# Kernel optimization log

Hardware: AMD Instinct MI355X
Metric: run time of the kernel (lower is better)

The kernel has to match this reference:

```python
import jax, jax.numpy as jnp
import numpy as np

D_MODEL, D_INNER, D_STATE, D_CONV = 1024, 2048, 16, 4
LN_EPS = 1e-5


def setup_inputs() -> dict:
    key = jax.random.key(0)
    ks = jax.random.split(key, 8)
    B, T = 2, 1024
    s = 0.02
    A = jnp.broadcast_to(jnp.arange(1, D_STATE + 1, dtype=jnp.float32), (D_INNER, D_STATE))
    return {
        "x": jax.random.normal(ks[0], (B, T, D_MODEL), jnp.float32),
        "ln_gamma": jnp.ones((D_MODEL,), jnp.float32),
        "ln_beta": jnp.zeros((D_MODEL,), jnp.float32),
        "W_in": jax.random.normal(ks[1], (2 * D_INNER, D_MODEL), jnp.float32) * s,
        "conv_w": jax.random.normal(ks[2], (D_INNER, D_CONV), jnp.float32) * s,
        "conv_b": jnp.zeros((D_INNER,), jnp.float32),
        "W_x": jax.random.normal(ks[3], (2 * D_STATE + 1, D_INNER), jnp.float32) * s,
        "w_dt": jax.random.normal(ks[4], (D_INNER, 1), jnp.float32) * s,
        "b_dt": jnp.zeros((D_INNER,), jnp.float32),
        "A_log": jnp.log(A),
        "D_param": jnp.ones((D_INNER,), jnp.float32),
        "W_out": jax.random.normal(ks[5], (D_MODEL, D_INNER), jnp.float32) * s,
    }


def _mamba_forward(x, ln_gamma, ln_beta, W_in, conv_w, conv_b, W_x, w_dt, b_dt, A_log, D_param, W_out):
    residual = x
    B, T, _ = x.shape
    # LayerNorm
    mu = x.mean(-1, keepdims=True)
    var = ((x - mu) ** 2).mean(-1, keepdims=True)
    xn = (x - mu) / jnp.sqrt(var + LN_EPS) * ln_gamma + ln_beta
    # in_proj -> split into x branch and gate z
    xz = xn @ W_in.T                       # [B,T,2*d_inner]
    xb, z = jnp.split(xz, 2, axis=-1)
    # depthwise causal conv1d (torch pad=d_conv-1, truncated to T == left pad)
    xp = jnp.pad(xb, ((0, 0), (D_CONV - 1, 0), (0, 0)))
    xc = conv_b + sum(xp[:, k:k + T, :] * conv_w[:, k] for k in range(D_CONV))
    xc = jax.nn.silu(xc)                   # [B,T,d_inner]
    # ssm parameter projections
    ssm_p = xc @ W_x.T                     # [B,T,2*d_state+1]
    dt_raw = ssm_p[..., :1]
    Bp = ssm_p[..., 1:1 + D_STATE]
    Cp = ssm_p[..., 1 + D_STATE:]
    dt = jax.nn.softplus(dt_raw @ w_dt.T + b_dt)   # [B,T,d_inner]
    A = -jnp.exp(A_log)                    # [d_inner,d_state]

    def step(h, inp):
        dt_t, x_t, B_t, C_t = inp          # [B,d], [B,d], [B,n], [B,n]
        A_bar = jnp.exp(dt_t[:, :, None] * A[None])          # [B,d,n]
        h = A_bar * h + (dt_t * x_t)[:, :, None] * B_t[:, None, :]
        y_t = jnp.einsum('bdn,bn->bd', h, C_t)
        return h, y_t

    h0 = jnp.zeros((B, D_INNER, D_STATE), x.dtype)
    xs = (jnp.swapaxes(dt, 0, 1), jnp.swapaxes(xc, 0, 1),
          jnp.swapaxes(Bp, 0, 1), jnp.swapaxes(Cp, 0, 1))
    _, ys = jax.lax.scan(step, h0, xs)     # ys: [T,B,d_inner]
    y = jnp.swapaxes(ys, 0, 1)
    y = y + D_param * xc
    y = y * jax.nn.silu(z)
    return residual + y @ W_out.T


def reference(x, ln_gamma, ln_beta, W_in, conv_w, conv_b, W_x, w_dt, b_dt, A_log, D_param, W_out):
    return _mamba_forward(x, ln_gamma, ln_beta, W_in, conv_w, conv_b, W_x, w_dt, b_dt, A_log, D_param, W_out)
```

## Files before the change

kernel.cpp:

```cpp
#include <hip/hip_runtime.h>
#include <hip/hip_bf16.h>

#define DM 1024
#define DI 2048
#define DS 16
#define DC 4
#define BB 2
#define TT 1024
#define MM (BB*TT)
#define CCH 32
#define LCH 32

typedef unsigned short u16;
typedef __attribute__((ext_vector_type(8))) short bf16x8;
typedef __attribute__((ext_vector_type(4))) float f32x4;

__device__ __forceinline__ float bu2f(u16 u) {
    union { unsigned int i; float f; } w; w.i = ((unsigned int)u) << 16; return w.f;
}
__device__ __forceinline__ u16 f2bu(float f) {
    union { float f; unsigned int u; } w; w.f = f;
    unsigned int r = w.u + 0x7fffu + ((w.u >> 16) & 1u);
    return (u16)(r >> 16);
}

#define F2B_BLOCKS 6144
__global__ __launch_bounds__(256) void prep_kernel(const float* __restrict__ x,
                                                   const float* __restrict__ gamma,
                                                   const float* __restrict__ beta,
                                                   u16* __restrict__ xn,
                                                   const float* __restrict__ Wi,
                                                   u16* __restrict__ Wi_b,
                                                   const float* __restrict__ Wo,
                                                   u16* __restrict__ Wo_b) {
    const int tid = threadIdx.x;
    if (blockIdx.x >= MM) {
        const int n4W = 2 * DI * DM / 4;
        int i = (blockIdx.x - MM) * 256 + tid;
        const float* in; u16* out;
        if (i < n4W) { in = Wi; out = Wi_b; }
        else { in = Wo; out = Wo_b; i -= n4W; }
        float4 v = reinterpret_cast<const float4*>(in)[i];
        ushort4 o;
        o.x = f2bu(v.x); o.y = f2bu(v.y); o.z = f2bu(v.z); o.w = f2bu(v.w);
        reinterpret_cast<ushort4*>(out)[i] = o;
        return;
    }
    __shared__ float sbuf[8];
    const int row = blockIdx.x;
    float4 v = reinterpret_cast<const float4*>(x + (size_t)row * DM)[tid];

    float s = v.x + v.y + v.z + v.w;
    #pragma unroll
    for (int off = 32; off; off >>= 1) s += __shfl_down(s, off);
    if ((tid & 63) == 0) sbuf[tid >> 6] = s;
    __syncthreads();
    float mu = (sbuf[0] + sbuf[1] + sbuf[2] + sbuf[3]) * (1.0f / DM);
    __syncthreads();

    float d0 = v.x - mu, d1 = v.y - mu, d2 = v.z - mu, d3 = v.w - mu;
    float q = d0*d0 + d1*d1 + d2*d2 + d3*d3;
    #pragma unroll
    for (int off = 32; off; off >>= 1) q += __shfl_down(q, off);
    if ((tid & 63) == 0) sbuf[tid >> 6] = q;
    __syncthreads();
    float var = (sbuf[0] + sbuf[1] + sbuf[2] + sbuf[3]) * (1.0f / DM);
    float rstd = rsqrtf(var + 1e-5f);

    float4 g = reinterpret_cast<const float4*>(gamma)[tid];
    float4 b = reinterpret_cast<const float4*>(beta)[tid];
    ushort4 o;
    o.x = f2bu(d0 * rstd * g.x + b.x);
    o.y = f2bu(d1 * rstd * g.y + b.y);
    o.z = f2bu(d2 * rstd * g.z + b.z);
    o.w = f2bu(d3 * rstd * g.w + b.w);
    reinterpret_cast<ushort4*>(xn + (size_t)row * DM)[tid] = o;
}

__device__ __forceinline__ void gl_lds(const u16* g, u16* lds) {
    __builtin_amdgcn_global_load_lds((const __attribute__((address_space(1))) void*)g,
                                     (__attribute__((address_space(3))) void*)lds,
                                     16, 0, 0);
}

__global__ __launch_bounds__(256) void gemm1_mfma(const u16* __restrict__ A,
                                                  const u16* __restrict__ B,
                                                  u16* __restrict__ C,
                                                  int M, int N, int K) {
    __shared__ u16 As[2][128 * 32];
    __shared__ u16 Bs[2][128 * 32];
    const int tid  = threadIdx.x;
    const int lane = tid & 63;
    const int w    = tid >> 6;
    const int wm   = (w >> 1) * 64, wn = (w & 1) * 64;
    const int m0   = blockIdx.y * 128, n0 = blockIdx.x * 128;

    const int srow = tid >> 2;
    const int sk   = (tid & 3) * 8;
    const u16* aP0 = A + (size_t)(m0 + srow) * K + sk;
    const u16* aP1 = aP0 + (size_t)64 * K;
    const u16* bP0 = B + (size_t)(n0 + srow) * K + sk;
    const u16* bP1 = bP0 + (size_t)64 * K;
    const int ldst = tid * 8;

    const int fr = lane & 15, fq = (lane >> 4) * 8;

    gl_lds(aP0, &As[0][ldst]); gl_lds(aP1, &As[0][2048 + ldst]);
    gl_lds(bP0, &Bs[0][ldst]); gl_lds(bP1, &Bs[0][2048 + ldst]);
    __syncthreads();

    const int iters = K >> 5;
    f32x4 acc[4][4] = {};
    for (int it = 0; it < iters; it++) {
        const int cur = it & 1;
        const int kn = (it + 1) << 5;
        if (kn < K) {
            const int nb = cur ^ 1;
            gl_lds(aP0 + kn, &As[nb][ldst]); gl_lds(aP1 + kn, &As[nb][2048 + ldst]);
            gl_lds(bP0 + kn, &Bs[nb][ldst]); gl_lds(bP1 + kn, &Bs[nb][2048 + ldst]);
        }
        bf16x8 af[4], bf[4];
        #pragma unroll
        for (int i = 0; i < 4; i++)
            af[i] = *reinterpret_cast<const bf16x8*>(&As[cur][(wm + i * 16 + fr) * 32 + fq]);
        #pragma unroll
        for (int j = 0; j < 4; j++)
            bf[j] = *reinterpret_cast<const bf16x8*>(&Bs[cur][(wn + j * 16 + fr) * 32 + fq]);
        #pragma unroll
        for (int i = 0; i < 4; i++)
            #pragma unroll
            for (int j = 0; j < 4; j++)
                acc[i][j] = __builtin_amdgcn_mfma_f32_16x16x32_bf16(af[i], bf[j], acc[i][j], 0, 0, 0);
        __syncthreads();
    }

    const int erow = (lane >> 4) * 4, ecol = lane & 15;
    #pragma unroll
    for (int i = 0; i < 4; i++)
        #pragma unroll
        for (int j = 0; j < 4; j++) {
            const int col = n0 + wn + j * 16 + ecol;
            #pragma unroll
            for (int r = 0; r < 4; r++) {
                const int row = m0 + wm + i * 16 + erow + r;
                C[(size_t)row * N + col] = f2bu(acc[i][j][r]);
            }
        }
}

__global__ __launch_bounds__(256) void gemm2_mfma(const u16* __restrict__ A,
                                                  const u16* __restrict__ B,
                                                  float* __restrict__ C,
                                                  const float* __restrict__ resid,
                                                  int M, int N, int K) {
    __shared__ u16 As[2][2][64 * 32];
    __shared__ u16 Bs[2][2][64 * 32];
    const int tid  = threadIdx.x;
    const int lane = tid & 63;
    const int w    = tid >> 6;
    const int wm   = (w >> 1) * 32, wn = (w & 1) * 32;
    const int m0   = blockIdx.y * 64, n0 = blockIdx.x * 64;

    const int srow = tid >> 2;
    const int sk   = (tid & 3) * 8;
    const u16* aP = A + (size_t)(m0 + srow) * K + sk;
    const u16* bP = B + (size_t)(n0 + srow) * K + sk;
    const int ldst = tid * 8;

    const int fr = lane & 15, fq = (lane >> 4) * 8;

    gl_lds(aP,      &As[0][0][ldst]); gl_lds(aP + 32, &As[0][1][ldst]);
    gl_lds(bP,      &Bs[0][0][ldst]); gl_lds(bP + 32, &Bs[0][1][ldst]);
    __syncthreads();

    const int iters = K >> 6;
    f32x4 acc[2][2] = {};
    for (int it = 0; it < iters; it++) {
        const int cur = it & 1;
        const int kn = (it + 1) << 6;
        if (kn < K) {
            const int nb = cur ^ 1;
            gl_lds(aP + kn,      &As[nb][0][ldst]); gl_lds(aP + kn + 32, &As[nb][1][ldst]);
            gl_lds(bP + kn,      &Bs[nb][0][ldst]); gl_lds(bP + kn + 32, &Bs[nb][1][ldst]);
        }
        #pragma unroll
        for (int kh = 0; kh < 2; kh++) {
            bf16x8 af[2], bf[2];
            #pragma unroll
            for (int i = 0; i < 2; i++)
                af[i] = *reinterpret_cast<const bf16x8*>(&As[cur][kh][(wm + i * 16 + fr) * 32 + fq]);
            #pragma unroll
            for (int j = 0; j < 2; j++)
                bf[j] = *reinterpret_cast<const bf16x8*>(&Bs[cur][kh][(wn + j * 16 + fr) * 32 + fq]);
            #pragma unroll
            for (int i = 0; i < 2; i++)
                #pragma unroll
                for (int j = 0; j < 2; j++)
                    acc[i][j] = __builtin_amdgcn_mfma_f32_16x16x32_bf16(af[i], bf[j], acc[i][j], 0, 0, 0);
        }
        __syncthreads();
    }

    const int erow = (lane >> 4) * 4, ecol = lane & 15;
    #pragma unroll
    for (int i = 0; i < 2; i++)
        #pragma unroll
        for (int j = 0; j < 2; j++) {
            const int col = n0 + wn + j * 16 + ecol;
            #pragma unroll
            for (int r = 0; r < 4; r++) {
                const int row = m0 + wm + i * 16 + erow + r;
                C[(size_t)row * N + col] = acc[i][j][r] + resid[(size_t)row * N + col];
            }
        }
}

__global__ __launch_bounds__(256) void convproj_kernel(const u16* __restrict__ xz,
                                                       const float* __restrict__ cw,
                                                       const float* __restrict__ cb,
                                                       const float* __restrict__ Wx,
                                                       u16* __restrict__ xc,
                                                       float* __restrict__ ssm) {
    __shared__ float xs[4][DI];
    const int tid  = threadIdx.x;
    const int row0 = blockIdx.x * 4;
    const int t0   = row0 & (TT - 1);
    const int d0   = tid * 8;

    float xv[7][8];
    #pragma unroll
    for (int j = 0; j < 7; j++) {
        const int tr = t0 - 3 + j;
        if (tr >= 0) {
            const uint4 v = *reinterpret_cast<const uint4*>(xz + (size_t)(row0 - 3 + j) * (2 * DI) + d0);
            unsigned int uu[4] = { v.x, v.y, v.z, v.w };
            #pragma unroll
            for (int e = 0; e < 4; e++) {
                union { unsigned int i; float f; } lo, hi;
                lo.i = (uu[e] & 0xffffu) << 16;
                hi.i = uu[e] & 0xffff0000u;
                xv[j][2 * e]     = lo.f;
                xv[j][2 * e + 1] = hi.f;
            }
        } else {
            #pragma unroll
            for (int e = 0; e < 8; e++) xv[j][e] = 0.f;
        }
    }

    float4 w4[8];
    #pragma unroll
    for (int e = 0; e < 8; e++) w4[e] = reinterpret_cast<const float4*>(cw)[d0 + e];
    float bias[8];
    *reinterpret_cast<float4*>(&bias[0]) = reinterpret_cast<const float4*>(cb + d0)[0];
    *reinterpret_cast<float4*>(&bias[4]) = reinterpret_cast<const float4*>(cb + d0)[1];

    #pragma unroll
    for (int r = 0; r < 4; r++) {
        u16 pk[8];
        #pragma unroll
        for (int e = 0; e < 8; e++) {
            float a = bias[e] + xv[r][e]     * w4[e].x + xv[r + 1][e] * w4[e].y
                              + xv[r + 2][e] * w4[e].z + xv[r + 3][e] * w4[e].w;
            float sv = a / (1.0f + __expf(-a));
            xs[r][d0 + e] = sv;
            pk[e] = f2bu(sv);
        }
        ushort4 o0 = make_ushort4(pk[0], pk[1], pk[2], pk[3]);
        ushort4 o1 = make_ushort4(pk[4], pk[5], pk[6], pk[7]);
        ushort4* outp = reinterpret_cast<ushort4*>(xc + (size_t)(row0 + r) * DI + d0);
        outp[0] = o0; outp[1] = o1;
    }
    __syncthreads();

    const int w = tid >> 6, lane = tid & 63;
    for (int n = w; n < 2 * DS + 1; n += 4) {
        const float* wr = Wx + (size_t)n * DI;
        float a0 = 0.f, a1 = 0.f, a2 = 0.f, a3 = 0.f;
        #pragma unroll 4
        for (int i = 0; i < DI / 64; i++) {
            float wv = wr[i * 64 + lane];
            a0 += wv * xs[0][i * 64 + lane];
            a1 += wv * xs[1][i * 64 + lane];
            a2 += wv * xs[2][i * 64 + lane];
            a3 += wv * xs[3][i * 64 + lane];
        }
        #pragma unroll
        for (int off = 32; off; off >>= 1) {
            a0 += __shfl_down(a0, off);
            a1 += __shfl_down(a1, off);
            a2 += __shfl_down(a2, off);
            a3 += __shfl_down(a3, off);
        }
        if (lane == 0) {
            ssm[(size_t)(row0 + 0) * 33 + n] = a0;
            ssm[(size_t)(row0 + 1) * 33 + n] = a1;
            ssm[(size_t)(row0 + 2) * 33 + n] = a2;
            ssm[(size_t)(row0 + 3) * 33 + n] = a3;
        }
    }
}

__global__ __launch_bounds__(256) void scan_part1(const float* __restrict__ ssm,
                                                  const u16* __restrict__ xcy,
                                                  const float* __restrict__ w_dt,
                                                  const float* __restrict__ b_dt,
                                                  const float* __restrict__ A_log,
                                                  float* __restrict__ F,
                                                  float* __restrict__ Sdt) {
    __shared__ float sm[LCH * 33];
    __shared__ u16 xls[LCH * 256];
    const int tid = threadIdx.x;
    const int dt8 = blockIdx.x & 7;
    const int bc  = blockIdx.x >> 3;
    const int c   = bc & (CCH - 1);
    const int b   = bc >> 5;
    const int d   = dt8 * 256 + tid;

    const int base = ((b * TT) + c * LCH) * 33;
    for (int i = tid; i < LCH * 33; i += 256) sm[i] = ssm[base + i];
    const u16* xg = xcy + (size_t)(b * TT + c * LCH) * DI + dt8 * 256;
    for (int i = tid; i < LCH * 128; i += 256) {
        int t = i >> 7, dp = i & 127;
        unsigned int v = *reinterpret_cast<const unsigned int*>(xg + (size_t)t * DI + dp * 2);
        *reinterpret_cast<unsigned int*>(&xls[t * 256 + dp * 2]) = v;
    }
    __syncthreads();

    float A[DS], h[DS];
    #pragma unroll
    for (int n = 0; n < DS; n++) { A[n] = -__expf(A_log[d * DS + n]); h[n] = 0.f; }
    const float wdt = w_dt[d], bdt = b_dt[d];
    float sdt = 0.f;

    for (int t = 0; t < LCH; t++) {
        const float* sp = &sm[t * 33];
        float pre = sp[0] * wdt + bdt;
        float dtv = (pre > 20.f) ? pre : __logf(1.f + __expf(pre));
        sdt += dtv;
        float xv = bu2f(xls[t * 256 + tid]);
        float u = dtv * xv;
        #pragma unroll
        for (int n = 0; n < DS; n++) h[n] = __expf(dtv * A[n]) * h[n] + u * sp[1 + n];
    }
    const size_t fo = ((size_t)(b * CCH + c) * DI + d) * DS;
    #pragma unroll
    for (int n = 0; n < DS; n++) F[fo + n] = h[n];
    Sdt[(b * CCH + c) * DI + d] = sdt;
}

__global__ __launch_bounds__(256) void scan_combine(float* __restrict__ F,
                                                    const float* __restrict__ Sdt,
                                                    const float* __restrict__ A_log) {
    const int g = blockIdx.x * 256 + threadIdx.x;
    const int n = g & (DS - 1);
    const int d = (g >> 4) & (DI - 1);
    const int b = g >> 15;
    const float A = -__expf(A_log[d * DS + n]);
    float h = 0.f;
    for (int c = 0; c < CCH; c++) {
        const size_t o = ((size_t)(b * CCH + c) * DI + d) * DS + n;
        float f = F[o];
        float q = __expf(Sdt[(b * CCH + c) * DI + d] * A);
        float hn = q * h + f;
        F[o] = h;
        h = hn;
    }
}

__global__ __launch_bounds__(256) void scan_part2(const float* __restrict__ ssm,
                                                  const u16* __restrict__ xz,
                                                  u16* __restrict__ xcy,
                                                  const float* __restrict__ w_dt,
                                                  const float* __restrict__ b_dt,
                                                  const float* __restrict__ A_log,
                                                  const float* __restrict__ Dp,
                                                  const float* __restrict__ Hin) {
    __shared__ float sm[LCH * 33];
    __shared__ u16 xls[LCH * 256];
    const int tid = threadIdx.x;
    const int dt8 = blockIdx.x & 7;
    const int bc  = blockIdx.x >> 3;
    const int c   = bc & (CCH - 1);
    const int b   = bc >> 5;
    const int d   = dt8 * 256 + tid;

    const int base = ((b * TT) + c * LCH) * 33;
    for (int i = tid; i < LCH * 33; i += 256) sm[i] = ssm[base + i];
    const u16* xg = xcy + (size_t)(b * TT + c * LCH) * DI + dt8 * 256;
    for (int i = tid; i < LCH * 128; i += 256) {
        int t = i >> 7, dp = i & 127;
        unsigned int v = *reinterpret_cast<const unsigned int*>(xg + (size_t)t * DI + dp * 2);
        *reinterpret_cast<unsigned int*>(&xls[t * 256 + dp * 2]) = v;
    }
    __syncthreads();

    float A[DS], h[DS];
    const size_t ho = ((size_t)(b * CCH + c) * DI + d) * DS;
    #pragma unroll
    for (int n = 0; n < DS; n++) { A[n] = -__expf(A_log[d * DS + n]); h[n] = Hin[ho + n]; }
    const float wdt = w_dt[d], bdt = b_dt[d], Dv = Dp[d];

    for (int t = 0; t < LCH; t++) {
        const float* sp = &sm[t * 33];
        float pre = sp[0] * wdt + bdt;
        float dtv = (pre > 20.f) ? pre : __logf(1.f + __expf(pre));
        const size_t row = (size_t)(b * TT + c * LCH + t);
        float xv = bu2f(xls[t * 256 + tid]);
        float u = dtv * xv;
        float y = 0.f;
        #pragma unroll
        for (int n = 0; n < DS; n++) {
            h[n] = __expf(dtv * A[n]) * h[n] + u * sp[1 + n];
            y += h[n] * sp[17 + n];
        }
        float z = bu2f(xz[row * (2 * DI) + DI + d]);
        float sz = z / (1.0f + __expf(-z));
        xcy[row * DI + d] = f2bu((y + Dv * xv) * sz);
    }
}

extern "C" void kernel_launch(void* const* d_in, const int* in_sizes, int n_in,
                              void* d_out, int out_size, void* d_ws, size_t ws_size,
                              hipStream_t stream) {
    int ix, ig, ib, iWin, icw, icb, iWx, iwdt, ibdt, iAl, iD, iWo;
    if (n_in >= 12 && in_sizes[0] == 32768) {
        iAl = 0; iD = 1; iWin = 2; iWo = 3; iWx = 4; ibdt = 5;
        icb = 6; icw = 7; ib = 8; ig = 9; iwdt = 10; ix = 11;
    } else if (n_in >= 12 && in_sizes[0] == 2097152 && in_sizes[1] == 2048 && in_sizes[2] == 32768) {
        iWo = 0; iD = 1; iAl = 2; ibdt = 3; iwdt = 4; iWx = 5;
        icb = 6; icw = 7; iWin = 8; ib = 9; ig = 10; ix = 11;
    } else {
        ix = 0; ig = 1; ib = 2; iWin = 3; icw = 4; icb = 5;
        iWx = 6; iwdt = 7; ibdt = 8; iAl = 9; iD = 10; iWo = 11;
    }

    const float* x       = (const float*)d_in[ix];
    const float* ln_g    = (const float*)d_in[ig];
    const float* ln_b    = (const float*)d_in[ib];
    const float* W_in    = (const float*)d_in[iWin];
    const float* conv_w  = (const float*)d_in[icw];
    const float* conv_b  = (const float*)d_in[icb];
    const float* W_x     = (const float*)d_in[iWx];
    const float* w_dt    = (const float*)d_in[iwdt];
    const float* b_dt    = (const float*)d_in[ibdt];
    const float* A_log   = (const float*)d_in[iAl];
    const float* D_param = (const float*)d_in[iD];
    const float* W_out   = (const float*)d_in[iWo];
    float* out = (float*)d_out;

    float* ssm  = (float*)d_ws;
    u16*   xn   = (u16*)(ssm + (size_t)MM * 33);
    u16*   xz   = xn + (size_t)MM * DM;
    u16*   xcy  = xz + (size_t)MM * 2 * DI;
    float* F    = (float*)(xcy + (size_t)MM * DI);
    float* Sdt  = F + (size_t)BB * CCH * DI * DS;
    u16*   Wi_b = (u16*)(Sdt + (size_t)BB * CCH * DI);
    u16*   Wo_b = Wi_b + (size_t)2 * DI * DM;

    prep_kernel<<<MM + F2B_BLOCKS, 256, 0, stream>>>(x, ln_g, ln_b, xn, W_in, Wi_b, W_out, Wo_b);

    gemm1_mfma<<<dim3(4096 / 128, MM / 128), 256, 0, stream>>>(xn, Wi_b, xz, MM, 2 * DI, DM);

    convproj_kernel<<<MM / 4, 256, 0, stream>>>(xz, conv_w, conv_b, W_x, xcy, ssm);

    scan_part1<<<BB * CCH * (DI / 256), 256, 0, stream>>>(ssm, xcy, w_dt, b_dt, A_log, F, Sdt);
    scan_combine<<<(BB * DI * DS) / 256, 256, 0, stream>>>(F, Sdt, A_log);
    scan_part2<<<BB * CCH * (DI / 256), 256, 0, stream>>>(ssm, xz, xcy, w_dt, b_dt, A_log, D_param, F);

    gemm2_mfma<<<dim3(1024 / 64, MM / 64), 256, 0, stream>>>(xcy, Wo_b, out, x, MM, DM, DI);
}
```

Baseline: 226.3 us.

## Compute conv x_proj with bf16 MFMA and process 8 rows per block

Converts W_x to bf16 in the prep kernel and replaces the scalar warp-reduction projection in convproj with 16x16x32 bf16 MFMA over a packed shared-memory tile. Each block now handles 8 time rows instead of 4, which halves the block count and reuses the overlapping conv halo loads. Partial sums from the four waves are reduced through shared memory. The projection now uses bf16 weights and activations, which lowers precision, and half of the MFMA rows are padding that does no useful work.

Measured after the change: 209.6 us. 1.08x faster.

```diff
diff --git a/kernel.cpp b/kernel.cpp
--- a/kernel.cpp
+++ b/kernel.cpp
@@ -10,6 +10,7 @@
 #define MM (BB*TT)
 #define CCH 32
 #define LCH 32
+#define PR 8
 
 typedef unsigned short u16;
 typedef __attribute__((ext_vector_type(8))) short bf16x8;
@@ -23,8 +24,16 @@
     unsigned int r = w.u + 0x7fffu + ((w.u >> 16) & 1u);
     return (u16)(r >> 16);
 }
-
-#define F2B_BLOCKS 6144
+__device__ __forceinline__ float upk(const uint4& v, int e) {
+    unsigned int u;
+    switch (e >> 1) { case 0: u = v.x; break; case 1: u = v.y; break;
+                      case 2: u = v.z; break; default: u = v.w; }
+    union { unsigned int i; float f; } w;
+    w.i = (e & 1) ? (u & 0xffff0000u) : (u << 16);
+    return w.f;
+}
+
+#define F2B_BLOCKS 6210
 __global__ __launch_bounds__(256) void prep_kernel(const float* __restrict__ x,
                                                    const float* __restrict__ gamma,
                                                    const float* __restrict__ beta,
@@ -32,14 +41,18 @@
                                                    const float* __restrict__ Wi,
                                                    u16* __restrict__ Wi_b,
                                                    const float* __restrict__ Wo,
-                                                   u16* __restrict__ Wo_b) {
+                                                   u16* __restrict__ Wo_b,
+                                                   const float* __restrict__ Wx,
+                                                   u16* __restrict__ Wx_b) {
     const int tid = threadIdx.x;
     if (blockIdx.x >= MM) {
-        const int n4W = 2 * DI * DM / 4;
+        const int n4W  = 2 * DI * DM / 4;
+        const int n4Wo = DM * DI / 4;
         int i = (blockIdx.x - MM) * 256 + tid;
         const float* in; u16* out;
         if (i < n4W) { in = Wi; out = Wi_b; }
-        else { in = Wo; out = Wo_b; i -= n4W; }
+        else if (i < n4W + n4Wo) { in = Wo; out = Wo_b; i -= n4W; }
+        else { in = Wx; out = Wx_b; i -= n4W + n4Wo; }
         float4 v = reinterpret_cast<const float4*>(in)[i];
         ushort4 o;
         o.x = f2bu(v.x); o.y = f2bu(v.y); o.z = f2bu(v.z); o.w = f2bu(v.w);
@@ -218,35 +231,15 @@
 __global__ __launch_bounds__(256) void convproj_kernel(const u16* __restrict__ xz,
                                                        const float* __restrict__ cw,
                                                        const float* __restrict__ cb,
-                                                       const float* __restrict__ Wx,
+                                                       const u16* __restrict__ Wxb,
                                                        u16* __restrict__ xc,
                                                        float* __restrict__ ssm) {
-    __shared__ float xs[4][DI];
+    __shared__ u16 xs[64 * PR * 32];
+    __shared__ float red[4][PR][48];
     const int tid  = threadIdx.x;
-    const int row0 = blockIdx.x * 4;
+    const int row0 = blockIdx.x * PR;
     const int t0   = row0 & (TT - 1);
     const int d0   = tid * 8;
-
-    float xv[7][8];
-    #pragma unroll
-    for (int j = 0; j < 7; j++) {
-        const int tr = t0 - 3 + j;
-        if (tr >= 0) {
-            const uint4 v = *reinterpret_cast<const uint4*>(xz + (size_t)(row0 - 3 + j) * (2 * DI) + d0);
-            unsigned int uu[4] = { v.x, v.y, v.z, v.w };
-            #pragma unroll
-            for (int e = 0; e < 4; e++) {
-                union { unsigned int i; float f; } lo, hi;
-                lo.i = (uu[e] & 0xffffu) << 16;
-                hi.i = uu[e] & 0xffff0000u;
-                xv[j][2 * e]     = lo.f;
-                xv[j][2 * e + 1] = hi.f;
-            }
-        } else {
-            #pragma unroll
-            for (int e = 0; e < 8; e++) xv[j][e] = 0.f;
-        }
-    }
 
     float4 w4[8];
     #pragma unroll
@@ -255,48 +248,70 @@
     *reinterpret_cast<float4*>(&bias[0]) = reinterpret_cast<const float4*>(cb + d0)[0];
     *reinterpret_cast<float4*>(&bias[4]) = reinterpret_cast<const float4*>(cb + d0)[1];
 
-    #pragma unroll
-    for (int r = 0; r < 4; r++) {
-        u16 pk[8];
+    uint4 pk[PR + 3];
+    #pragma unroll
+    for (int j = 0; j < PR + 3; j++) {
+        const int tr = t0 - 3 + j;
+        if (tr >= 0)
+            pk[j] = *reinterpret_cast<const uint4*>(xz + (size_t)(row0 - 3 + j) * (2 * DI) + d0);
+        else
+            pk[j] = make_uint4(0, 0, 0, 0);
+    }
+
+    const int kt_w = tid >> 2;
+    const int ko_w = (tid & 3) * 8;
+    #pragma unroll
+    for (int r = 0; r < PR; r++) {
+        u16 ob[8];
         #pragma unroll
         for (int e = 0; e < 8; e++) {
-            float a = bias[e] + xv[r][e]     * w4[e].x + xv[r + 1][e] * w4[e].y
-                              + xv[r + 2][e] * w4[e].z + xv[r + 3][e] * w4[e].w;
+            float a = bias[e]
+                    + upk(pk[r],     e) * w4[e].x
+                    + upk(pk[r + 1], e) * w4[e].y
+                    + upk(pk[r + 2], e) * w4[e].z
+                    + upk(pk[r + 3], e) * w4[e].w;
             float sv = a / (1.0f + __expf(-a));
-            xs[r][d0 + e] = sv;
-            pk[e] = f2bu(sv);
-        }
-        ushort4 o0 = make_ushort4(pk[0], pk[1], pk[2], pk[3]);
-        ushort4 o1 = make_ushort4(pk[4], pk[5], pk[6], pk[7]);
-        ushort4* outp = reinterpret_cast<ushort4*>(xc + (size_t)(row0 + r) * DI + d0);
-        outp[0] = o0; outp[1] = o1;
-    }
-    __syncthreads();
-
-    const int w = tid >> 6, lane = tid & 63;
-    for (int n = w; n < 2 * DS + 1; n += 4) {
-        const float* wr = Wx + (size_t)n * DI;
-        float a0 = 0.f, a1 = 0.f, a2 = 0.f, a3 = 0.f;
-        #pragma unroll 4
-        for (int i = 0; i < DI / 64; i++) {
-            float wv = wr[i * 64 + lane];
-            a0 += wv * xs[0][i * 64 + lane];
-            a1 += wv * xs[1][i * 64 + lane];
-            a2 += wv * xs[2][i * 64 + lane];
-            a3 += wv * xs[3][i * 64 + lane];
-        }
-        #pragma unroll
-        for (int off = 32; off; off >>= 1) {
-            a0 += __shfl_down(a0, off);
-            a1 += __shfl_down(a1, off);
-            a2 += __shfl_down(a2, off);
-            a3 += __shfl_down(a3, off);
-        }
-        if (lane == 0) {
-            ssm[(size_t)(row0 + 0) * 33 + n] = a0;
-            ssm[(size_t)(row0 + 1) * 33 + n] = a1;
-            ssm[(size_t)(row0 + 2) * 33 + n] = a2;
-            ssm[(size_t)(row0 + 3) * 33 + n] = a3;
+            ob[e] = f2bu(sv);
+        }
+        uint4 o;
+        o.x = (unsigned)ob[0] | ((unsigned)ob[1] << 16);
+        o.y = (unsigned)ob[2] | ((unsigned)ob[3] << 16);
+        o.z = (unsigned)ob[4] | ((unsigned)ob[5] << 16);
+        o.w = (unsigned)ob[6] | ((unsigned)ob[7] << 16);
+        *reinterpret_cast<uint4*>(xc + (size_t)(row0 + r) * DI + d0) = o;
+        *reinterpret_cast<uint4*>(&xs[kt_w * (PR * 32) + r * 32 + ko_w]) = o;
+    }
+    __syncthreads();
+
+    const int lane = tid & 63, w = tid >> 6;
+    const int fr = lane & 15, fq = (lane >> 4) * 8;
+    f32x4 acc[3] = {};
+    const int kt0 = w * 16;
+    #pragma unroll 4
+    for (int kt = kt0; kt < kt0 + 16; kt++) {
+        bf16x8 af = *reinterpret_cast<const bf16x8*>(&xs[kt * (PR * 32) + (fr & 7) * 32 + fq]);
+        #pragma unroll
+        for (int j = 0; j < 3; j++) {
+            int bn = j * 16 + fr; if (bn > 32) bn = 32;
+            bf16x8 bf = *reinterpret_cast<const bf16x8*>(Wxb + (size_t)bn * DI + kt * 32 + fq);
+            acc[j] = __builtin_amdgcn_mfma_f32_16x16x32_bf16(af, bf, acc[j], 0, 0, 0);
+        }
+    }
+    const int erow = (lane >> 4) * 4, ecol = lane & 15;
+    if (erow < PR) {
+        #pragma unroll
+        for (int j = 0; j < 3; j++)
+            #pragma unroll
+            for (int r = 0; r < 4; r++)
+                red[w][erow + r][j * 16 + ecol] = acc[j][r];
+    }
+    __syncthreads();
+
+    if (tid < PR * 48) {
+        const int rr = tid / 48, n = tid % 48;
+        if (n < 33) {
+            float s = red[0][rr][n] + red[1][rr][n] + red[2][rr][n] + red[3][rr][n];
+            ssm[(size_t)(row0 + rr) * 33 + n] = s;
         }
     }
 }
@@ -457,12 +472,14 @@
     float* Sdt  = F + (size_t)BB * CCH * DI * DS;
     u16*   Wi_b = (u16*)(Sdt + (size_t)BB * CCH * DI);
     u16*   Wo_b = Wi_b + (size_t)2 * DI * DM;
-
-    prep_kernel<<<MM + F2B_BLOCKS, 256, 0, stream>>>(x, ln_g, ln_b, xn, W_in, Wi_b, W_out, Wo_b);
+    u16*   Wx_b = Wo_b + (size_t)DM * DI;
+
+    prep_kernel<<<MM + F2B_BLOCKS, 256, 0, stream>>>(x, ln_g, ln_b, xn, W_in, Wi_b,
+                                                     W_out, Wo_b, W_x, Wx_b);
 
     gemm1_mfma<<<dim3(4096 / 128, MM / 128), 256, 0, stream>>>(xn, Wi_b, xz, MM, 2 * DI, DM);
 
-    convproj_kernel<<<MM / 4, 256, 0, stream>>>(xz, conv_w, conv_b, W_x, xcy, ssm);
+    convproj_kernel<<<MM / PR, 256, 0, stream>>>(xz, conv_w, conv_b, Wx_b, xcy, ssm);
 
     scan_part1<<<BB * CCH * (DI / 256), 256, 0, stream>>>(ssm, xcy, w_dt, b_dt, A_log, F, Sdt);
     scan_combine<<<(BB * DI * DS) / 256, 256, 0, stream>>>(F, Sdt, A_log);
```
